# Kernel tuning notes

Measured on AMD Instinct MI355X. Metric: run time of the kernel, lower is better.

Reference implementation:

```python
import jax, jax.numpy as jnp
import numpy as np

B, LQ, LK, E, H, NF, NE, HID = 4, 8192, 8192, 256, 8, 2, 4, 256


def _split(x, h):
    b, l, e = x.shape
    return x.reshape(b, l, h, e // h).transpose(0, 2, 1, 3)  # (B,H,L,D)


def _merge(x):
    b, h, l, d = x.shape
    return x.transpose(0, 2, 1, 3).reshape(b, l, h * d)


def _experts(x, W1, b1, W2, b2, W3, b3):
    # x: (B,N,in); W*: (E, out, in). Returns (E,B,N,out). Exact (erf) GELU as torch.
    h = jax.nn.gelu(jnp.einsum('bni,ehi->ebnh', x, W1) + b1[:, None, None, :], approximate=False)
    h = jax.nn.gelu(jnp.einsum('ebnh,egh->ebng', h, W2) + b2[:, None, None, :], approximate=False)
    return jnp.einsum('ebng,eog->ebno', h, W3) + b3[:, None, None, :]


def _combine(expert_out, scores):
    # expert_out: (E,B,N,out); scores: (B,N,1,E) -> (B,N,out)
    return jnp.einsum('ebno,bne->bno', expert_out, scores[:, :, 0, :])


def _forward(scores, query, input_functions,
             ca_Wq, ca_bq, ca_Wk, ca_bk, ca_Wv, ca_bv, ca_Wo, ca_bo,
             sa_Wq, sa_bq, sa_Wk, sa_bk, sa_Wv, sa_bv, sa_Wo, sa_bo,
             f1_W1, f1_b1, f1_W2, f1_b2, f1_W3, f1_b3,
             f2_W1, f2_b1, f2_W2, f2_b2, f2_W3, f2_b3):
    h = H
    # ---- cross attention over NF input functions ----
    q = jax.nn.softmax(_split(query @ ca_Wq.T + ca_bq, h), -1)  # (B,H,Lq,D)
    k = jnp.einsum('fble,fde->fbld', input_functions, ca_Wk) + ca_bk[:, None, None, :]
    v = jnp.einsum('fble,fde->fbld', input_functions, ca_Wv) + ca_bv[:, None, None, :]
    f, b, lk, e = k.shape
    d = e // h
    k = jax.nn.softmax(k.reshape(f, b, lk, h, d).transpose(0, 1, 3, 2, 4), -1)  # (F,B,H,Lk,D)
    v = v.reshape(f, b, lk, h, d).transpose(0, 1, 3, 2, 4)
    k_sum = k.sum(3, keepdims=True)                       # (F,B,H,1,D)
    alpha = 1.0 / (q[None] * k_sum).sum(-1, keepdims=True)  # (F,B,H,Lq,1)
    tmp = jnp.einsum('fbhld,fbhlv->fbhdv', k, v)          # (F,B,H,D,D)
    out = (alpha * jnp.einsum('bhld,fbhdv->fbhlv', q, tmp)).mean(0)  # (B,H,Lq,D)
    ca = (_merge(q) + _merge(out)) @ ca_Wo.T + ca_bo
    # expert FFN1 + score-weighted combine, residual
    query = query + _combine(_experts(ca, f1_W1, f1_b1, f1_W2, f1_b2, f1_W3, f1_b3), scores)
    # ---- self attention ----
    q2 = jax.nn.softmax(_split(query @ sa_Wq.T + sa_bq, h), -1)
    k2 = jax.nn.softmax(_split(query @ sa_Wk.T + sa_bk, h), -1)
    v2 = _split(query @ sa_Wv.T + sa_bv, h)
    k_sum2 = k2.sum(2, keepdims=True)
    alpha2 = 1.0 / (q2 * k_sum2).sum(-1, keepdims=True)
    tmp2 = jnp.einsum('bhld,bhlv->bhdv', k2, v2)
    out2 = alpha2 * jnp.einsum('bhld,bhdv->bhlv', q2, tmp2)
    sa = (_merge(q2) + _merge(out2)) @ sa_Wo.T + sa_bo
    query = query + _combine(_experts(sa, f2_W1, f2_b1, f2_W2, f2_b2, f2_W3, f2_b3), scores)
    return query


def setup_inputs() -> dict:
    ks = iter(jax.random.split(jax.random.key(0), 64))
    def p(shape):
        return jax.random.normal(next(ks), shape, jnp.float32) * 0.02
    inp = {
        'scores': jax.random.uniform(next(ks), (B, LQ, 1, NE), jnp.float32),
        'query': jax.random.normal(next(ks), (B, LQ, E), jnp.float32),
        'input_functions': jax.random.normal(next(ks), (NF, B, LK, E), jnp.float32),
        'ca_Wq': p((E, E)), 'ca_bq': p((E,)),
        'ca_Wk': p((NF, E, E)), 'ca_bk': p((NF, E)),
        'ca_Wv': p((NF, E, E)), 'ca_bv': p((NF, E)),
        'ca_Wo': p((E, E)), 'ca_bo': p((E,)),
        'sa_Wq': p((E, E)), 'sa_bq': p((E,)),
        'sa_Wk': p((E, E)), 'sa_bk': p((E,)),
        'sa_Wv': p((E, E)), 'sa_bv': p((E,)),
        'sa_Wo': p((E, E)), 'sa_bo': p((E,)),
        'f1_W1': p((NE, HID, E)), 'f1_b1': p((NE, HID)),
        'f1_W2': p((NE, HID, HID)), 'f1_b2': p((NE, HID)),
        'f1_W3': p((NE, HID, HID)), 'f1_b3': p((NE, HID)),
        'f2_W1': p((NE, HID, E)), 'f2_b1': p((NE, HID)),
        'f2_W2': p((NE, HID, HID)), 'f2_b2': p((NE, HID)),
        'f2_W3': p((NE, HID, HID)), 'f2_b3': p((NE, HID)),
    }
    return inp


def reference(scores, query, input_functions,
              ca_Wq, ca_bq, ca_Wk, ca_bk, ca_Wv, ca_bv, ca_Wo, ca_bo,
              sa_Wq, sa_bq, sa_Wk, sa_bk, sa_Wv, sa_bv, sa_Wo, sa_bo,
              f1_W1, f1_b1, f1_W2, f1_b2, f1_W3, f1_b3,
              f2_W1, f2_b1, f2_W2, f2_b2, f2_W3, f2_b3):
    return _forward(scores, query, input_functions,
                    ca_Wq, ca_bq, ca_Wk, ca_bk, ca_Wv, ca_bv, ca_Wo, ca_bo,
                    sa_Wq, sa_bq, sa_Wk, sa_bk, sa_Wv, sa_bv, sa_Wo, sa_bo,
                    f1_W1, f1_b1, f1_W2, f1_b2, f1_W3, f1_b3,
                    f2_W1, f2_b1, f2_W2, f2_b2, f2_W3, f2_b3)
```

## Files before the change

### kernel.cpp

```cpp
#include <hip/hip_runtime.h>


typedef unsigned short u16;
typedef __attribute__((ext_vector_type(8))) short   bs8;
typedef __attribute__((ext_vector_type(4))) float   f32x4;
typedef __attribute__((ext_vector_type(16))) float  f32x16;

__device__ __forceinline__ float bf2f(u16 u) {
  union { float f; unsigned i; } c; c.i = ((unsigned)u) << 16; return c.f;
}
__device__ __forceinline__ u16 f2bf(float f) {
  union { float f; unsigned i; } c; c.f = f;
  unsigned x = c.i;
  return (u16)((x + 0x7fffu + ((x >> 16) & 1u)) >> 16);
}
__device__ __forceinline__ unsigned pack2(float a, float b) {
  return (unsigned)f2bf(a) | ((unsigned)f2bf(b) << 16);
}
__device__ __forceinline__ float gelu_f(float x) {
  const float t = x * (0.7978845608f + 0.0356774081f * x * x);
  return x / (1.f + __expf(-2.f * t));
}

#define EPI_PLAIN 0
#define EPI_QSM   4

template <bool AF32, int EPI>
__global__ __launch_bounds__(256, 2) void gemm256(
    const void* __restrict__ Ain, const u16* __restrict__ W,
    const float* __restrict__ bias, u16* __restrict__ outb) {
  __shared__ int4 ash[1024];
  __shared__ int4 wsh[1024];
  const int tid = threadIdx.x;
  const int m0 = blockIdx.x * 128, n0 = blockIdx.y * 128;
  const int wave = tid >> 6, lane = tid & 63;
  const int wm = (wave >> 1) * 64, wn = (wave & 1) * 64;
  const int lr = lane & 15, lk = lane >> 4;
  f32x4 acc[4][4];
#pragma unroll
  for (int m = 0; m < 4; ++m)
#pragma unroll
    for (int n = 0; n < 4; ++n) acc[m][n] = f32x4{0.f, 0.f, 0.f, 0.f};

  const float* Af = (const float*)Ain;
  const u16*   Ab = (const u16*)Ain;

  for (int kt = 0; kt < 4; ++kt) {
    const int k0 = kt * 64;
    if (kt) __syncthreads();
#pragma unroll
    for (int it = 0; it < 4; ++it) {
      const int s = tid + it * 256;
      const int row = s >> 3, c16 = s & 7;
      const int dst = (row << 3) | (c16 ^ (row & 7));
      const long src = (long)(m0 + row) * 256 + k0 + c16 * 8;
      int4 val;
      if constexpr (AF32) {
        const float4* p = (const float4*)(Af + src);
        const float4 x = p[0], y = p[1];
        val.x = pack2(x.x, x.y); val.y = pack2(x.z, x.w);
        val.z = pack2(y.x, y.y); val.w = pack2(y.z, y.w);
      } else {
        val = *(const int4*)(Ab + src);
      }
      ash[dst] = val;
    }
#pragma unroll
    for (int it = 0; it < 4; ++it) {
      const int s = tid + it * 256;
      const int row = s >> 3, c16 = s & 7;
      const int dst = (row << 3) | (c16 ^ (row & 7));
      wsh[dst] = *(const int4*)(W + (long)(n0 + row) * 256 + k0 + c16 * 8);
    }
    __syncthreads();
#pragma unroll
    for (int kk = 0; kk < 2; ++kk) {
      bs8 af[4], wf[4];
#pragma unroll
      for (int m = 0; m < 4; ++m) {
        const int row = wm + m * 16 + lr;
        af[m] = *(const bs8*)&ash[(row << 3) | ((kk * 4 + lk) ^ (row & 7))];
      }
#pragma unroll
      for (int n = 0; n < 4; ++n) {
        const int row = wn + n * 16 + lr;
        wf[n] = *(const bs8*)&wsh[(row << 3) | ((kk * 4 + lk) ^ (row & 7))];
      }
#pragma unroll
      for (int m = 0; m < 4; ++m)
#pragma unroll
        for (int n = 0; n < 4; ++n)
          acc[m][n] = __builtin_amdgcn_mfma_f32_16x16x32_bf16(af[m], wf[n],
                                                              acc[m][n], 0, 0, 0);
    }
  }
  if constexpr (EPI == EPI_QSM) {
#pragma unroll
    for (int m = 0; m < 4; ++m) {
      const int rb = m0 + wm + m * 16 + lk * 4;
#pragma unroll
      for (int j = 0; j < 4; ++j) {
#pragma unroll
        for (int hh = 0; hh < 2; ++hh) {
          const int c0 = n0 + wn + (2 * hh) * 16 + lr;
          const float p0 = __expf(acc[m][2 * hh][j] + bias[c0]);
          const float p1 = __expf(acc[m][2 * hh + 1][j] + bias[c0 + 16]);
          float s = p0 + p1;
#pragma unroll
          for (int o = 8; o >= 1; o >>= 1) s += __shfl_xor(s, o);
          const float inv = 1.0f / s;
          outb[(long)(rb + j) * 256 + c0]      = f2bf(p0 * inv);
          outb[(long)(rb + j) * 256 + c0 + 16] = f2bf(p1 * inv);
        }
      }
    }
  } else {
#pragma unroll
    for (int m = 0; m < 4; ++m) {
      const int rb = m0 + wm + m * 16 + lk * 4;
#pragma unroll
      for (int n = 0; n < 4; ++n) {
        const int gc = n0 + wn + n * 16 + lr;
        const float bv = bias[gc];
#pragma unroll
        for (int j = 0; j < 4; ++j)
          outb[(long)(rb + j) * 256 + gc] = f2bf(acc[m][n][j] + bv);
      }
    }
  }
}

__global__ __launch_bounds__(512, 4) void ffn4(
    const u16* __restrict__ X, const u16* __restrict__ Wbase,
    int w1slot, int w2slot, int w3slot,
    const float* __restrict__ b1, const float* __restrict__ b2,
    const float* __restrict__ b3, const float* __restrict__ scores,
    const float* __restrict__ csrc, float* __restrict__ outf) {
  __shared__ int4 xsh[2048];
  __shared__ int4 hsh[2048];
  __shared__ int4 wsh[1024];
  const int tid = threadIdx.x, wave = tid >> 6, lane = tid & 63;
  const int wm = (wave >> 2) * 32, wn = (wave & 3) * 64;
  const int lr = lane & 15, lk = lane >> 4;
  const long m0 = (long)blockIdx.x * 64;

#pragma unroll
  for (int it = 0; it < 4; ++it) {
    const int s = tid + it * 512;
    const int row = s >> 5, c8 = s & 31;
    const int cs = (c8 & 24) | ((c8 ^ row) & 7);
    xsh[row * 32 + cs] = *(const int4*)(X + (m0 + row) * 256 + c8 * 8);
  }

  f32x4 oacc[2][4];
#pragma unroll
  for (int m = 0; m < 2; ++m)
#pragma unroll
    for (int n = 0; n < 4; ++n) oacc[m][n] = f32x4{0.f, 0.f, 0.f, 0.f};
  f32x4 acc[2][4];

  for (int e = 0; e < 4; ++e) {
#pragma unroll 1
    for (int l = 0; l < 3; ++l) {
      const int slot = (l == 0 ? w1slot : (l == 1 ? w2slot : w3slot)) + e;
      const u16* Wl = Wbase + (long)slot * 65536;
      const int4* asrc = (l == 0) ? xsh : hsh;
#pragma unroll
      for (int m = 0; m < 2; ++m)
#pragma unroll
        for (int n = 0; n < 4; ++n) acc[m][n] = f32x4{0.f, 0.f, 0.f, 0.f};
      for (int kt = 0; kt < 8; ++kt) {
        __syncthreads();
#pragma unroll
        for (int it = 0; it < 2; ++it) {
          const int s = tid + it * 512;
          const int row = s >> 2, c4 = s & 3;
          wsh[row * 4 + (c4 ^ (row & 3))] =
              *(const int4*)(Wl + (long)row * 256 + kt * 32 + c4 * 8);
        }
        __syncthreads();
        bs8 af[2], wf[4];
        const int c8 = kt * 4 + lk;
#pragma unroll
        for (int m = 0; m < 2; ++m) {
          const int row = wm + m * 16 + lr;
          const int cs = (c8 & 24) | ((c8 ^ row) & 7);
          af[m] = *(const bs8*)&asrc[row * 32 + cs];
        }
#pragma unroll
        for (int n = 0; n < 4; ++n) {
          const int row = wn + n * 16 + lr;
          wf[n] = *(const bs8*)&wsh[row * 4 + ((lk ^ row) & 3)];
        }
#pragma unroll
        for (int m = 0; m < 2; ++m)
#pragma unroll
          for (int n = 0; n < 4; ++n)
            acc[m][n] = __builtin_amdgcn_mfma_f32_16x16x32_bf16(
                af[m], wf[n], acc[m][n], 0, 0, 0);
      }
      __syncthreads();
      if (l < 2) {
        const float* bb = (l == 0 ? b1 : b2) + e * 256;
        u16* hp = (u16*)hsh;
#pragma unroll
        for (int m = 0; m < 2; ++m)
#pragma unroll
          for (int n = 0; n < 4; ++n) {
            const int col = wn + n * 16 + lr;
            const float bv = bb[col];
            const int c8w = col >> 3;
#pragma unroll
            for (int j = 0; j < 4; ++j) {
              const int row = wm + m * 16 + lk * 4 + j;
              const int cs = (c8w & 24) | ((c8w ^ row) & 7);
              hp[row * 256 + cs * 8 + (col & 7)] =
                  f2bf(gelu_f(acc[m][n][j] + bv));
            }
          }
      } else {
#pragma unroll
        for (int m = 0; m < 2; ++m) {
#pragma unroll
          for (int j = 0; j < 4; ++j) {
            const float sc = scores[(m0 + wm + m * 16 + lk * 4 + j) * 4 + e];
#pragma unroll
            for (int n = 0; n < 4; ++n)
              oacc[m][n][j] +=
                  sc * (acc[m][n][j] + b3[e * 256 + wn + n * 16 + lr]);
          }
        }
      }
    }
  }
#pragma unroll
  for (int m = 0; m < 2; ++m) {
#pragma unroll
    for (int n = 0; n < 4; ++n) {
      const int col = wn + n * 16 + lr;
#pragma unroll
      for (int j = 0; j < 4; ++j) {
        const long idx = (m0 + wm + m * 16 + lk * 4 + j) * 256 + col;
        outf[idx] = csrc[idx] + oacc[m][n][j];
      }
    }
  }
}

__global__ __launch_bounds__(1024, 4) void kvstats(
    const float* __restrict__ Ain, const u16* __restrict__ Wk,
    const u16* __restrict__ Wv, const float* __restrict__ bk,
    const float* __restrict__ bv, float* __restrict__ pks,
    float* __restrict__ ptm) {
  __shared__ __align__(16) char smem[73728];
  int4* ash  = (int4*)smem;
  int4* wksh = ash + 512;
  int4* wvsh = wksh + 2048;
  u16* KnT = (u16*)smem;
  u16* VT  = KnT + 256 * 72;
  const int tid = threadIdx.x;
  const int wave = tid >> 6, lane = tid & 63;
  const int lr = lane & 15, lk = lane >> 4;
  const int kvsel = wave >> 3, w3 = wave & 7;
  const int wm = (w3 >> 2) * 32, wn = (w3 & 3) * 64;
  const int b = blockIdx.y, ch = blockIdx.x;
  const long r0 = (long)b * 8192 + (long)ch * 64;

  f32x4 acc[2][4];
#pragma unroll
  for (int m = 0; m < 2; ++m)
#pragma unroll
    for (int n = 0; n < 4; ++n) acc[m][n] = f32x4{0.f, 0.f, 0.f, 0.f};

  for (int kt = 0; kt < 4; ++kt) {
    const int k0 = kt * 64;
    if (kt) __syncthreads();
    if (tid < 512) {
      const int row = tid >> 3, c16 = tid & 7;
      const int dst = (row << 3) | (c16 ^ (row & 7));
      const float4* p = (const float4*)(Ain + (r0 + row) * 256 + k0 + c16 * 8);
      const float4 x = p[0], y = p[1];
      int4 val;
      val.x = pack2(x.x, x.y); val.y = pack2(x.z, x.w);
      val.z = pack2(y.x, y.y); val.w = pack2(y.z, y.w);
      ash[dst] = val;
    }
#pragma unroll
    for (int it = 0; it < 2; ++it) {
      const int s = tid + it * 1024;
      const int row = s >> 3, c16 = s & 7;
      const int dst = (row << 3) | (c16 ^ (row & 7));
      wksh[dst] = *(const int4*)(Wk + (long)row * 256 + k0 + c16 * 8);
      wvsh[dst] = *(const int4*)(Wv + (long)row * 256 + k0 + c16 * 8);
    }
    __syncthreads();
    const int4* wsh = kvsel ? wvsh : wksh;
#pragma unroll
    for (int kk = 0; kk < 2; ++kk) {
      bs8 af[2], wf[4];
#pragma unroll
      for (int m = 0; m < 2; ++m) {
        const int row = wm + m * 16 + lr;
        af[m] = *(const bs8*)&ash[(row << 3) | ((kk * 4 + lk) ^ (row & 7))];
      }
#pragma unroll
      for (int n = 0; n < 4; ++n) {
        const int row = wn + n * 16 + lr;
        wf[n] = *(const bs8*)&wsh[(row << 3) | ((kk * 4 + lk) ^ (row & 7))];
      }
#pragma unroll
      for (int m = 0; m < 2; ++m)
#pragma unroll
        for (int n = 0; n < 4; ++n)
          acc[m][n] = __builtin_amdgcn_mfma_f32_16x16x32_bf16(af[m], wf[n],
                                                              acc[m][n], 0, 0, 0);
    }
  }
  __syncthreads();

  const float* bias = kvsel ? bv : bk;
  if (kvsel == 0) {
#pragma unroll
    for (int m = 0; m < 2; ++m)
#pragma unroll
      for (int j = 0; j < 4; ++j)
#pragma unroll
        for (int hh = 0; hh < 2; ++hh) {
          const int c0 = wn + (2 * hh) * 16 + lr;
          const float p0 = __expf(acc[m][2 * hh][j] + bias[c0]);
          const float p1 = __expf(acc[m][2 * hh + 1][j] + bias[c0 + 16]);
          float s = p0 + p1;
#pragma unroll
          for (int o = 8; o >= 1; o >>= 1) s += __shfl_xor(s, o);
          const float inv = 1.0f / s;
          acc[m][2 * hh][j] = p0 * inv;
          acc[m][2 * hh + 1][j] = p1 * inv;
        }
  }
  {
    u16* T = kvsel ? VT : KnT;
#pragma unroll
    for (int m = 0; m < 2; ++m) {
      const int rb = wm + m * 16 + lk * 4;
#pragma unroll
      for (int n = 0; n < 4; ++n) {
        const int col = wn + n * 16 + lr;
        float v0 = acc[m][n][0], v1 = acc[m][n][1];
        float v2 = acc[m][n][2], v3 = acc[m][n][3];
        if (kvsel) {
          const float bb = bias[col];
          v0 += bb; v1 += bb; v2 += bb; v3 += bb;
        }
        uint2 w;
        w.x = pack2(v0, v1); w.y = pack2(v2, v3);
        *(uint2*)(T + col * 72 + rb) = w;
      }
    }
  }
  __syncthreads();

  if (kvsel == 0) {
    const int h = w3;
    f32x16 aT, aK;
#pragma unroll
    for (int r = 0; r < 16; ++r) { aT[r] = 0.f; aK[r] = 0.f; }
    bs8 ones;
#pragma unroll
    for (int e = 0; e < 8; ++e) ones[e] = (short)0x3F80;
    const u16* kcol = KnT + (h * 32 + (lane & 31)) * 72;
    const u16* vcol = VT  + (h * 32 + (lane & 31)) * 72;
    const int hi8 = (lane >> 5) * 8;
#pragma unroll
    for (int ks = 0; ks < 4; ++ks) {
      const bs8 a  = *(const bs8*)(kcol + ks * 16 + hi8);
      const bs8 vb = *(const bs8*)(vcol + ks * 16 + hi8);
      aT = __builtin_amdgcn_mfma_f32_32x32x16_bf16(vb, a, aT, 0, 0, 0);
      aK = __builtin_amdgcn_mfma_f32_32x32x16_bf16(a, ones, aK, 0, 0, 0);
    }
    const long blk = (long)b * gridDim.x + ch;
    float* po = ptm + blk * 8192 + h * 1024;
#pragma unroll
    for (int r = 0; r < 16; ++r) {
      const int dv = (r & 3) + 8 * (r >> 2) + 4 * (lane >> 5);
      po[dv * 32 + (lane & 31)] = aT[r];
    }
    if ((lane & 31) == 0) {
#pragma unroll
      for (int r = 0; r < 16; ++r) {
        const int dk = (r & 3) + 8 * (r >> 2) + 4 * (lane >> 5);
        pks[blk * 256 + h * 32 + dk] = aK[r];
      }
    }
  }
}

__global__ void reduceStats(const float* __restrict__ pk,
                            const float* __restrict__ pt,
                            float* __restrict__ ksum, float* __restrict__ tmp) {
  const int b = blockIdx.y;
  const int i = blockIdx.x * 256 + threadIdx.x;
  float s = 0.f;
  if (i < 256) {
    const float* p = pk + (long)b * 128 * 256 + i;
    for (int c = 0; c < 128; ++c) s += p[c * 256];
    ksum[(long)b * 256 + i] = s;
  } else {
    const int j = i - 256;
    const float* p = pt + (long)b * 128 * 8192 + j;
    for (int c = 0; c < 128; ++c) s += p[c * 8192];
    tmp[(long)b * 8192 + j] = s;
  }
}

template <int F>
__global__ __launch_bounds__(256, 2) void mixk(const u16* __restrict__ q,
                                               const float* __restrict__ ksum,
                                               const float* __restrict__ tmp,
                                               u16* __restrict__ out) {
  constexpr int LF = (F == 2) ? 1 : 0;
  constexpr int QS = 264;
  __shared__ u16 qsh[64 * QS];
  __shared__ float alsh[64][17];
  __shared__ float ksh[8][F * 36];
  const int t = threadIdx.x;
  const int h = t >> 5, dv = t & 31;
  const int b = blockIdx.y;
  const long row0 = (long)b * 8192 + (long)blockIdx.x * 64;

#pragma unroll
  for (int it = 0; it < 8; ++it) {
    const int i = t + it * 256;
    const int r = i >> 5, c = i & 31;
    *(int4*)&qsh[r * QS + c * 8] = *(const int4*)&q[(row0 + r) * 256 + c * 8];
  }
#pragma unroll
  for (int f = 0; f < F; ++f)
    ksh[h][f * 36 + dv] = ksum[((long)f * 4 + b) * 256 + t];
  float tr[F][32];
#pragma unroll
  for (int f = 0; f < F; ++f) {
    const float* tp = tmp + ((long)f * 4 + b) * 8192 + h * 1024 + dv * 32;
#pragma unroll
    for (int c = 0; c < 8; ++c) {
      const float4 v = *(const float4*)(tp + c * 4);
      tr[f][c * 4] = v.x; tr[f][c * 4 + 1] = v.y;
      tr[f][c * 4 + 2] = v.z; tr[f][c * 4 + 3] = v.w;
    }
  }
  __syncthreads();

  for (int d = t; d < 64 * 8 * F; d += 256) {
    const int f = d & (F - 1);
    const int hh = (d >> LF) & 7;
    const int r = d >> (3 + LF);
    const u16* qp = &qsh[r * QS + hh * 32];
    const float* kp = &ksh[hh][f * 36];
    float s = 0.f;
#pragma unroll
    for (int c = 0; c < 4; ++c) {
      const bs8 qa = *(const bs8*)(qp + c * 8);
#pragma unroll
      for (int j = 0; j < 8; ++j) s += bf2f((u16)qa[j]) * kp[c * 8 + j];
    }
    alsh[r][(hh << LF) | f] = 1.0f / s;
  }
  __syncthreads();

#pragma unroll 2
  for (int r = 0; r < 64; ++r) {
    float qr[32];
    const u16* qp = &qsh[r * QS + h * 32];
#pragma unroll
    for (int c = 0; c < 4; ++c) {
      const bs8 qa = *(const bs8*)(qp + c * 8);
#pragma unroll
      for (int j = 0; j < 8; ++j) qr[c * 8 + j] = bf2f((u16)qa[j]);
    }
    float acc = 0.f;
#pragma unroll
    for (int f = 0; f < F; ++f) {
      float s0 = 0.f, s1 = 0.f;
#pragma unroll
      for (int dk = 0; dk < 32; dk += 2) {
        s0 += qr[dk] * tr[f][dk];
        s1 += qr[dk + 1] * tr[f][dk + 1];
      }
      acc += (s0 + s1) * alsh[r][(h << LF) | f];
    }
    const float qv = bf2f(qsh[r * QS + t]);
    out[(row0 + r) * 256 + t] = f2bf(qv + acc * (1.0f / (float)F));
  }
}

struct WTab { const float* p[34]; };
__global__ void convW(WTab tab, u16* __restrict__ dst) {
  const int s = blockIdx.y;
  const long i = ((long)blockIdx.x * 256 + threadIdx.x) * 4;
  const float4 v = *(const float4*)(tab.p[s] + i);
  ushort4 o;
  o.x = f2bf(v.x); o.y = f2bf(v.y); o.z = f2bf(v.z); o.w = f2bf(v.w);
  *(ushort4*)(dst + (long)s * 65536 + i) = o;
}

extern "C" void kernel_launch(void* const* d_in, const int* in_sizes, int n_in,
                              void* d_out, int out_size, void* d_ws, size_t ws_size,
                              hipStream_t stream) {
  (void)in_sizes; (void)n_in; (void)out_size; (void)ws_size;
  const float* scores = (const float*)d_in[0];
  const float* query  = (const float*)d_in[1];
  const float* IF     = (const float*)d_in[2];
  const float* ca_Wq = (const float*)d_in[3];  const float* ca_bq = (const float*)d_in[4];
  const float* ca_Wk = (const float*)d_in[5];  const float* ca_bk = (const float*)d_in[6];
  const float* ca_Wv = (const float*)d_in[7];  const float* ca_bv = (const float*)d_in[8];
  const float* ca_Wo = (const float*)d_in[9];  const float* ca_bo = (const float*)d_in[10];
  const float* sa_Wq = (const float*)d_in[11]; const float* sa_bq = (const float*)d_in[12];
  const float* sa_Wk = (const float*)d_in[13]; const float* sa_bk = (const float*)d_in[14];
  const float* sa_Wv = (const float*)d_in[15]; const float* sa_bv = (const float*)d_in[16];
  const float* sa_Wo = (const float*)d_in[17]; const float* sa_bo = (const float*)d_in[18];
  const float* f1W1 = (const float*)d_in[19]; const float* f1b1 = (const float*)d_in[20];
  const float* f1W2 = (const float*)d_in[21]; const float* f1b2 = (const float*)d_in[22];
  const float* f1W3 = (const float*)d_in[23]; const float* f1b3 = (const float*)d_in[24];
  const float* f2W1 = (const float*)d_in[25]; const float* f2b1 = (const float*)d_in[26];
  const float* f2W2 = (const float*)d_in[27]; const float* f2b2 = (const float*)d_in[28];
  const float* f2W3 = (const float*)d_in[29]; const float* f2b3 = (const float*)d_in[30];

  char* ws = (char*)d_ws;
  u16* X0 = (u16*)(ws);
  u16* X1 = (u16*)(ws + 16777216);
  u16* X2 = (u16*)(ws + 33554432);
  float* ptmX3 = (float*)(ws + 50331648);
  u16* W16 = (u16*)(ws + 67108864);
  float* ksum = (float*)(ws + 71565312);
  float* tmpb = (float*)(ws + 71573504);
  float* pks  = (float*)(ws + 71835648);
  float* qacc = (float*)d_out;

  WTab tab;
  tab.p[0] = ca_Wq; tab.p[1] = ca_Wk; tab.p[2] = ca_Wk + 65536;
  tab.p[3] = ca_Wv; tab.p[4] = ca_Wv + 65536; tab.p[5] = ca_Wo;
  tab.p[6] = sa_Wq; tab.p[7] = sa_Wk; tab.p[8] = sa_Wv; tab.p[9] = sa_Wo;
  for (int e = 0; e < 4; ++e) {
    tab.p[10 + e] = f1W1 + e * 65536; tab.p[14 + e] = f1W2 + e * 65536;
    tab.p[18 + e] = f1W3 + e * 65536; tab.p[22 + e] = f2W1 + e * 65536;
    tab.p[26 + e] = f2W2 + e * 65536; tab.p[30 + e] = f2W3 + e * 65536;
  }
  convW<<<dim3(64, 34), 256, 0, stream>>>(tab, W16);

  const dim3 gg(256, 2), gb(256);
  const dim3 kvg(128, 4), kvb(1024);
  gemm256<true, EPI_QSM><<<gg, gb, 0, stream>>>(query, W16 + 0 * 65536L, ca_bq, X0);
  for (int f = 0; f < 2; ++f) {
    kvstats<<<kvg, kvb, 0, stream>>>(IF + (long)f * 8388608,
                                     W16 + (1 + f) * 65536L, W16 + (3 + f) * 65536L,
                                     ca_bk + f * 256, ca_bv + f * 256, pks, ptmX3);
    reduceStats<<<dim3(33, 4), 256, 0, stream>>>(pks, ptmX3, ksum + f * 4 * 256, tmpb + (long)f * 4 * 8192);
  }
  mixk<2><<<dim3(128, 4), 256, 0, stream>>>(X0, ksum, tmpb, X1);
  gemm256<false, EPI_PLAIN><<<gg, gb, 0, stream>>>(X1, W16 + 5 * 65536L, ca_bo, X2);
  ffn4<<<512, 512, 0, stream>>>(X2, W16, 10, 14, 18, f1b1, f1b2, f1b3, scores, query, qacc);
  gemm256<true, EPI_QSM><<<gg, gb, 0, stream>>>(qacc, W16 + 6 * 65536L, sa_bq, X0);
  kvstats<<<kvg, kvb, 0, stream>>>(qacc, W16 + 7 * 65536L, W16 + 8 * 65536L,
                                   sa_bk, sa_bv, pks, ptmX3);
  reduceStats<<<dim3(33, 4), 256, 0, stream>>>(pks, ptmX3, ksum, tmpb);
  mixk<1><<<dim3(128, 4), 256, 0, stream>>>(X0, ksum, tmpb, X1);
  gemm256<false, EPI_PLAIN><<<gg, gb, 0, stream>>>(X1, W16 + 9 * 65536L, sa_bo, X2);
  ffn4<<<512, 512, 0, stream>>>(X2, W16, 22, 26, 30, f2b1, f2b2, f2b3, scores, qacc, qacc);
}
```

Baseline: 449.8 us.

## Pre-swizzle expert weights into MFMA fragment order and load directly from global

Expert FFN weights are converted into a layout where each lane's bs8 MFMA B-fragment is contiguous, so ffn4 reads weight fragments straight from global/L2 instead of staging them through shared memory. This removes the per-k-tile shared-memory store and two barriers per iteration, and unrolls the k loop. In exchange every block reloads the weights from cache with no LDS reuse across waves, which could increase L2 traffic and latency exposure.

```diff
diff --git a/kernel.cpp b/kernel.cpp
--- a/kernel.cpp
+++ b/kernel.cpp
@@ -131,16 +131,15 @@
 }
 
 __global__ __launch_bounds__(512, 4) void ffn4(
-    const u16* __restrict__ X, const u16* __restrict__ Wbase,
-    int w1slot, int w2slot, int w3slot,
+    const u16* __restrict__ X, const u16* __restrict__ WX, int wbase,
     const float* __restrict__ b1, const float* __restrict__ b2,
     const float* __restrict__ b3, const float* __restrict__ scores,
     const float* __restrict__ csrc, float* __restrict__ outf) {
   __shared__ int4 xsh[2048];
   __shared__ int4 hsh[2048];
-  __shared__ int4 wsh[1024];
   const int tid = threadIdx.x, wave = tid >> 6, lane = tid & 63;
-  const int wm = (wave >> 2) * 32, wn = (wave & 3) * 64;
+  const int wm = (wave >> 2) * 32, wn3 = wave & 3;
+  const int wn = wn3 * 64;
   const int lr = lane & 15, lk = lane >> 4;
   const long m0 = (long)blockIdx.x * 64;
 
@@ -151,6 +150,7 @@
     const int cs = (c8 & 24) | ((c8 ^ row) & 7);
     xsh[row * 32 + cs] = *(const int4*)(X + (m0 + row) * 256 + c8 * 8);
   }
+  __syncthreads();
 
   f32x4 oacc[2][4];
 #pragma unroll
@@ -162,23 +162,14 @@
   for (int e = 0; e < 4; ++e) {
 #pragma unroll 1
     for (int l = 0; l < 3; ++l) {
-      const int slot = (l == 0 ? w1slot : (l == 1 ? w2slot : w3slot)) + e;
-      const u16* Wl = Wbase + (long)slot * 65536;
+      const u16* wp = WX + (long)(wbase + l * 4 + e) * 65536 + (long)lane * 8;
       const int4* asrc = (l == 0) ? xsh : hsh;
 #pragma unroll
       for (int m = 0; m < 2; ++m)
 #pragma unroll
         for (int n = 0; n < 4; ++n) acc[m][n] = f32x4{0.f, 0.f, 0.f, 0.f};
+#pragma unroll
       for (int kt = 0; kt < 8; ++kt) {
-        __syncthreads();
-#pragma unroll
-        for (int it = 0; it < 2; ++it) {
-          const int s = tid + it * 512;
-          const int row = s >> 2, c4 = s & 3;
-          wsh[row * 4 + (c4 ^ (row & 3))] =
-              *(const int4*)(Wl + (long)row * 256 + kt * 32 + c4 * 8);
-        }
-        __syncthreads();
         bs8 af[2], wf[4];
         const int c8 = kt * 4 + lk;
 #pragma unroll
@@ -188,10 +179,8 @@
           af[m] = *(const bs8*)&asrc[row * 32 + cs];
         }
 #pragma unroll
-        for (int n = 0; n < 4; ++n) {
-          const int row = wn + n * 16 + lr;
-          wf[n] = *(const bs8*)&wsh[row * 4 + ((lk ^ row) & 3)];
-        }
+        for (int n = 0; n < 4; ++n)
+          wf[n] = *(const bs8*)(wp + ((kt * 16 + wn3 * 4 + n) << 9));
 #pragma unroll
         for (int m = 0; m < 2; ++m)
 #pragma unroll
@@ -199,8 +188,8 @@
             acc[m][n] = __builtin_amdgcn_mfma_f32_16x16x32_bf16(
                 af[m], wf[n], acc[m][n], 0, 0, 0);
       }
-      __syncthreads();
       if (l < 2) {
+        __syncthreads();
         const float* bb = (l == 0 ? b1 : b2) + e * 256;
         u16* hp = (u16*)hsh;
 #pragma unroll
@@ -218,6 +207,7 @@
                   f2bf(gelu_f(acc[m][n][j] + bv));
             }
           }
+        __syncthreads();
       } else {
 #pragma unroll
         for (int m = 0; m < 2; ++m) {
@@ -492,14 +482,30 @@
   }
 }
 
-struct WTab { const float* p[34]; };
-__global__ void convW(WTab tab, u16* __restrict__ dst) {
+struct WTab10 { const float* p[10]; };
+__global__ void convW(WTab10 tab, u16* __restrict__ dst) {
   const int s = blockIdx.y;
   const long i = ((long)blockIdx.x * 256 + threadIdx.x) * 4;
   const float4 v = *(const float4*)(tab.p[s] + i);
   ushort4 o;
   o.x = f2bf(v.x); o.y = f2bf(v.y); o.z = f2bf(v.z); o.w = f2bf(v.w);
   *(ushort4*)(dst + (long)s * 65536 + i) = o;
+}
+
+struct WTab24 { const float* p[24]; };
+__global__ void convWX(WTab24 tab, u16* __restrict__ dst) {
+  const int s = blockIdx.y;
+  const int o8 = blockIdx.x * 256 + threadIdx.x;
+  const int kt = o8 >> 10, nt = (o8 >> 6) & 15, lane = o8 & 63;
+  const int row = nt * 16 + (lane & 15);
+  const int col = kt * 32 + (lane >> 4) * 8;
+  const float* src = tab.p[s] + row * 256 + col;
+  const float4 a = *(const float4*)src;
+  const float4 b = *(const float4*)(src + 4);
+  int4 val;
+  val.x = pack2(a.x, a.y); val.y = pack2(a.z, a.w);
+  val.z = pack2(b.x, b.y); val.w = pack2(b.z, b.w);
+  *(int4*)(dst + (long)s * 65536 + (long)o8 * 8) = val;
 }
 
 extern "C" void kernel_launch(void* const* d_in, const int* in_sizes, int n_in,
@@ -530,21 +536,28 @@
   u16* X2 = (u16*)(ws + 33554432);
   float* ptmX3 = (float*)(ws + 50331648);
   u16* W16 = (u16*)(ws + 67108864);
+  u16* WX  = (u16*)(ws + 68419584);
   float* ksum = (float*)(ws + 71565312);
   float* tmpb = (float*)(ws + 71573504);
   float* pks  = (float*)(ws + 71835648);
   float* qacc = (float*)d_out;
 
-  WTab tab;
+  WTab10 tab;
   tab.p[0] = ca_Wq; tab.p[1] = ca_Wk; tab.p[2] = ca_Wk + 65536;
   tab.p[3] = ca_Wv; tab.p[4] = ca_Wv + 65536; tab.p[5] = ca_Wo;
   tab.p[6] = sa_Wq; tab.p[7] = sa_Wk; tab.p[8] = sa_Wv; tab.p[9] = sa_Wo;
+  convW<<<dim3(64, 10), 256, 0, stream>>>(tab, W16);
+
+  WTab24 tabx;
   for (int e = 0; e < 4; ++e) {
-    tab.p[10 + e] = f1W1 + e * 65536; tab.p[14 + e] = f1W2 + e * 65536;
-    tab.p[18 + e] = f1W3 + e * 65536; tab.p[22 + e] = f2W1 + e * 65536;
-    tab.p[26 + e] = f2W2 + e * 65536; tab.p[30 + e] = f2W3 + e * 65536;
-  }
-  convW<<<dim3(64, 34), 256, 0, stream>>>(tab, W16);
+    tabx.p[0 + e]  = f1W1 + e * 65536;
+    tabx.p[4 + e]  = f1W2 + e * 65536;
+    tabx.p[8 + e]  = f1W3 + e * 65536;
+    tabx.p[12 + e] = f2W1 + e * 65536;
+    tabx.p[16 + e] = f2W2 + e * 65536;
+    tabx.p[20 + e] = f2W3 + e * 65536;
+  }
+  convWX<<<dim3(32, 24), 256, 0, stream>>>(tabx, WX);
 
   const dim3 gg(256, 2), gb(256);
   const dim3 kvg(128, 4), kvb(1024);
@@ -557,12 +570,12 @@
   }
   mixk<2><<<dim3(128, 4), 256, 0, stream>>>(X0, ksum, tmpb, X1);
   gemm256<false, EPI_PLAIN><<<gg, gb, 0, stream>>>(X1, W16 + 5 * 65536L, ca_bo, X2);
-  ffn4<<<512, 512, 0, stream>>>(X2, W16, 10, 14, 18, f1b1, f1b2, f1b3, scores, query, qacc);
+  ffn4<<<512, 512, 0, stream>>>(X2, WX, 0, f1b1, f1b2, f1b3, scores, query, qacc);
   gemm256<true, EPI_QSM><<<gg, gb, 0, stream>>>(qacc, W16 + 6 * 65536L, sa_bq, X0);
   kvstats<<<kvg, kvb, 0, stream>>>(qacc, W16 + 7 * 65536L, W16 + 8 * 65536L,
                                    sa_bk, sa_bv, pks, ptmX3);
   reduceStats<<<dim3(33, 4), 256, 0, stream>>>(pks, ptmX3, ksum, tmpb);
   mixk<1><<<dim3(128, 4), 256, 0, stream>>>(X0, ksum, tmpb, X1);
   gemm256<false, EPI_PLAIN><<<gg, gb, 0, stream>>>(X1, W16 + 9 * 65536L, sa_bo, X2);
-  ffn4<<<512, 512, 0, stream>>>(X2, W16, 22, 26, 30, f2b1, f2b2, f2b3, scores, qacc, qacc);
-}
+  ffn4<<<512, 512, 0, stream>>>(X2, WX, 12, f2b1, f2b2, f2b3, scores, qacc, qacc);
+}
```

Measured after the change: 525.4 us. 1.17x slower.
